# Performance work log

Hardware: AMD Instinct MI355X
Metric: run time of the kernel (lower is better)

## Reference

```python
import jax, jax.numpy as jnp
import numpy as np

L, H = 16384, 1024

def setup_inputs() -> dict:
    key = jax.random.key(0)
    x = jax.random.normal(key, (L, H), dtype=jnp.float32)
    # learned parameter: tau initialized to log(0.8) per channel
    tau = jnp.full((H,), jnp.log(jnp.float32(0.8)), dtype=jnp.float32)
    return {"x": x, "tau": tau}

def _binop(q_i, q_j):
    # diagonal linear recurrence combine: x_j = A_j * x_i + b_j
    A_i, b_i = q_i
    A_j, b_j = q_j
    return (A_j * A_i, A_j * b_i + b_j)

def reference(x, tau):
    # Lambda_bar = exp(tau), B_bar = I  => Bu_elements = x
    Lambda_bar = jnp.exp(tau)                         # (H,)
    B_bar = jnp.eye(x.shape[1], dtype=x.dtype)        # (H, H) identity, as in original
    Bu = jnp.einsum('ph,lh->lp', B_bar, x)            # (L, H) == x
    Lambda_elements = jnp.broadcast_to(Lambda_bar, x.shape)  # (L, H)
    _, xs = jax.lax.associative_scan(_binop, (Lambda_elements, Bu))
    return xs  # (L, H)
```

## Files before the change

kernel.cpp:

```cpp
#include <hip/hip_runtime.h>
#include <cmath>


static constexpr int TC = 16;
static constexpr int P  = 16;

typedef float nt4 __attribute__((ext_vector_type(4)));

__global__ __launch_bounds__(256)
void li_ends(const float4* __restrict__ xv, const float4* __restrict__ tauv,
             float4* __restrict__ ends, int HV) {
    const int t = threadIdx.x;
    const int c = blockIdx.x;
    const float4 tv = tauv[t];
    const float lx = expf(tv.x), ly = expf(tv.y),
                lz = expf(tv.z), lw = expf(tv.w);

    const float4* xp = xv + (size_t)c * TC * HV + t;
    float4 buf[TC];
#pragma unroll
    for (int i = 0; i < TC; ++i)
        buf[i] = xp[(size_t)i * HV];

    float4 s = make_float4(0.f, 0.f, 0.f, 0.f);
#pragma unroll
    for (int i = 0; i < TC; ++i) {
        s.x = fmaf(lx, s.x, buf[i].x);
        s.y = fmaf(ly, s.y, buf[i].y);
        s.z = fmaf(lz, s.z, buf[i].z);
        s.w = fmaf(lw, s.w, buf[i].w);
    }
    ends[(size_t)c * HV + t] = s;
}

__global__ __launch_bounds__(256)
void li_pagg(const float4* __restrict__ ends, const float4* __restrict__ tauv,
             float4* __restrict__ pa, int HV) {
    const int gid = blockIdx.x * 256 + threadIdx.x;
    const int t = gid % HV;
    const int p = gid / HV;
    const float4 tv = tauv[t];
    const float Tx = expf(tv.x * (float)TC), Ty = expf(tv.y * (float)TC),
                Tz = expf(tv.z * (float)TC), Tw = expf(tv.w * (float)TC);

    const float4* ep = ends + (size_t)p * P * HV + t;
    float4 buf[P];
#pragma unroll
    for (int j = 0; j < P; ++j)
        buf[j] = ep[(size_t)j * HV];

    float4 s = make_float4(0.f, 0.f, 0.f, 0.f);
#pragma unroll
    for (int j = 0; j < P; ++j) {
        s.x = fmaf(Tx, s.x, buf[j].x);
        s.y = fmaf(Ty, s.y, buf[j].y);
        s.z = fmaf(Tz, s.z, buf[j].z);
        s.w = fmaf(Tw, s.w, buf[j].w);
    }
    pa[(size_t)p * HV + t] = s;
}

__global__ __launch_bounds__(256)
void li_pscan(float4* __restrict__ pa, const float4* __restrict__ tauv,
              int HV, int NP) {
    const int t = threadIdx.x;
    const float4 tv = tauv[t];
    const float fP = (float)(P * TC);
    const float Px = expf(tv.x * fP), Py = expf(tv.y * fP),
                Pz = expf(tv.z * fP), Pw = expf(tv.w * fP);
    float4 c = make_float4(0.f, 0.f, 0.f, 0.f);
    for (int p0 = 0; p0 < NP; p0 += 16) {
        float4 v[16];
#pragma unroll
        for (int j = 0; j < 16; ++j)
            v[j] = pa[(size_t)(p0 + j) * HV + t];
#pragma unroll
        for (int j = 0; j < 16; ++j) {
            const float4 a = v[j];
            v[j] = c;
            c.x = fmaf(Px, c.x, a.x);
            c.y = fmaf(Py, c.y, a.y);
            c.z = fmaf(Pz, c.z, a.z);
            c.w = fmaf(Pw, c.w, a.w);
        }
#pragma unroll
        for (int j = 0; j < 16; ++j)
            pa[(size_t)(p0 + j) * HV + t] = v[j];
    }
}

__global__ __launch_bounds__(256)
void li_out(const float4* __restrict__ xv, const float4* __restrict__ tauv,
            const float4* __restrict__ ends, const float4* __restrict__ pc,
            float4* __restrict__ yv, int HV) {
    const int t = threadIdx.x;
    const int c = blockIdx.x;
    const int p = c / P;
    const int r = c % P;
    const float4 tv = tauv[t];
    const float lx = expf(tv.x), ly = expf(tv.y),
                lz = expf(tv.z), lw = expf(tv.w);
    const float Tx = expf(tv.x * (float)TC), Ty = expf(tv.y * (float)TC),
                Tz = expf(tv.z * (float)TC), Tw = expf(tv.w * (float)TC);

    float4 carry = pc[(size_t)p * HV + t];
    {
        float4 v[P - 1];
        const float4* ep = ends + (size_t)p * P * HV + t;
#pragma unroll
        for (int j = 0; j < P - 1; ++j)
            if (j < r) v[j] = ep[(size_t)j * HV];
#pragma unroll
        for (int j = 0; j < P - 1; ++j) {
            if (j < r) {
                carry.x = fmaf(Tx, carry.x, v[j].x);
                carry.y = fmaf(Ty, carry.y, v[j].y);
                carry.z = fmaf(Tz, carry.z, v[j].z);
                carry.w = fmaf(Tw, carry.w, v[j].w);
            }
        }
    }

    const size_t base = (size_t)c * TC * HV + t;
    float4 buf[TC];
#pragma unroll
    for (int i = 0; i < TC; ++i)
        buf[i] = xv[base + (size_t)i * HV];

    float4 s = carry;
#pragma unroll
    for (int i = 0; i < TC; ++i) {
        s.x = fmaf(lx, s.x, buf[i].x);
        s.y = fmaf(ly, s.y, buf[i].y);
        s.z = fmaf(lz, s.z, buf[i].z);
        s.w = fmaf(lw, s.w, buf[i].w);
        buf[i] = s;
    }
    nt4* yn = (nt4*)yv;
#pragma unroll
    for (int i = 0; i < TC; ++i) {
        nt4 o = { buf[i].x, buf[i].y, buf[i].z, buf[i].w };
        __builtin_nontemporal_store(o, &yn[base + (size_t)i * HV]);
    }
}

extern "C" void kernel_launch(void* const* d_in, const int* in_sizes, int n_in,
                              void* d_out, int out_size, void* d_ws, size_t ws_size,
                              hipStream_t stream) {
    const float* x   = (const float*)d_in[0];
    const float* tau = (const float*)d_in[1];
    float* y = (float*)d_out;

    const int H  = in_sizes[1];
    const int L  = in_sizes[0] / H;
    const int C  = L / TC;
    const int NP = C / P;
    const int HV = H / 4;

    float4* ends = (float4*)d_ws;
    float4* pa   = ends + (size_t)C * HV;

    const float4* xv   = (const float4*)x;
    const float4* tauv = (const float4*)tau;

    li_ends <<<dim3(C),             dim3(256), 0, stream>>>(xv, tauv, ends, HV);
    li_pagg <<<dim3(NP * HV / 256), dim3(256), 0, stream>>>(ends, tauv, pa, HV);
    li_pscan<<<dim3(1),             dim3(256), 0, stream>>>(pa, tauv, HV, NP);
    li_out  <<<dim3(C),             dim3(256), 0, stream>>>(xv, tauv, ends, pa,
                                                            (float4*)y, HV);
}
```

Before: 132.7 us.

## Fuse scan stages into one cooperative kernel with register-resident chunk data

Replaces the four-kernel pipeline with one cooperative kernel that loads each x chunk once, keeps its local prefix in registers, and uses two grid-wide syncs between the chunk-end, partition-aggregate and output phases. The serial single-block partition scan is replaced by each block summing its preceding partition aggregates directly, and the output is formed as local prefix plus decayed carry, so x is not read a second time. C is 1024 blocks, and the cooperative launch needs all of them resident at once (256 CUs × 4 blocks). If that is not possible it falls back to the old kernels. The costs are grid-sync overhead and redundant carry work that grows with partition index.

```diff
diff --git a/kernel.cpp b/kernel.cpp
--- a/kernel.cpp
+++ b/kernel.cpp
@@ -1,11 +1,131 @@
 #include <hip/hip_runtime.h>
+#include <hip/hip_cooperative_groups.h>
 #include <cmath>
 
+
+namespace cg = cooperative_groups;
 
 static constexpr int TC = 16;
 static constexpr int P  = 16;
 
 typedef float nt4 __attribute__((ext_vector_type(4)));
+
+__device__ inline float4 ntload(const float4* p) {
+    nt4 v = __builtin_nontemporal_load((const nt4*)p);
+    return make_float4(v.x, v.y, v.z, v.w);
+}
+
+__global__ __launch_bounds__(256, 4)
+void li_coop(const float4* __restrict__ xv, const float4* __restrict__ tauv,
+             float4* __restrict__ yv, float4* __restrict__ ends,
+             float4* __restrict__ pa, int HV, int NP)
+{
+    const int t = threadIdx.x;
+    const int c = blockIdx.x;
+
+    const float4 tv = tauv[t];
+    const float lx = expf(tv.x), ly = expf(tv.y),
+                lz = expf(tv.z), lw = expf(tv.w);
+    const float Tx = expf(tv.x * (float)TC), Ty = expf(tv.y * (float)TC),
+                Tz = expf(tv.z * (float)TC), Tw = expf(tv.w * (float)TC);
+    const float fQ = (float)(TC * P);
+    const float Qx = expf(tv.x * fQ), Qy = expf(tv.y * fQ),
+                Qz = expf(tv.z * fQ), Qw = expf(tv.w * fQ);
+
+    const size_t base = (size_t)c * TC * HV + t;
+    float4 buf[TC];
+#pragma unroll
+    for (int i = 0; i < TC; ++i)
+        buf[i] = ntload(&xv[base + (size_t)i * HV]);
+
+    float4 s = make_float4(0.f, 0.f, 0.f, 0.f);
+#pragma unroll
+    for (int i = 0; i < TC; ++i) {
+        s.x = fmaf(lx, s.x, buf[i].x);
+        s.y = fmaf(ly, s.y, buf[i].y);
+        s.z = fmaf(lz, s.z, buf[i].z);
+        s.w = fmaf(lw, s.w, buf[i].w);
+        buf[i] = s;
+    }
+    ends[(size_t)c * HV + t] = s;
+
+    cg::this_grid().sync();
+
+    if (c < NP) {
+        const float4* ep = ends + (size_t)c * P * HV + t;
+        float4 a = make_float4(0.f, 0.f, 0.f, 0.f);
+#pragma unroll
+        for (int j0 = 0; j0 < P; j0 += 8) {
+            float4 v[8];
+#pragma unroll
+            for (int j = 0; j < 8; ++j)
+                v[j] = ep[(size_t)(j0 + j) * HV];
+#pragma unroll
+            for (int j = 0; j < 8; ++j) {
+                a.x = fmaf(Tx, a.x, v[j].x);
+                a.y = fmaf(Ty, a.y, v[j].y);
+                a.z = fmaf(Tz, a.z, v[j].z);
+                a.w = fmaf(Tw, a.w, v[j].w);
+            }
+        }
+        pa[(size_t)c * HV + t] = a;
+    }
+
+    cg::this_grid().sync();
+
+    const int p = c / P;
+    const int r = c % P;
+
+    float4 carry = make_float4(0.f, 0.f, 0.f, 0.f);
+    for (int q0 = 0; q0 < p; q0 += 8) {
+        const int n = p - q0;
+        float4 v[8];
+#pragma unroll
+        for (int j = 0; j < 8; ++j)
+            if (j < n) v[j] = pa[(size_t)(q0 + j) * HV + t];
+#pragma unroll
+        for (int j = 0; j < 8; ++j) {
+            if (j < n) {
+                carry.x = fmaf(Qx, carry.x, v[j].x);
+                carry.y = fmaf(Qy, carry.y, v[j].y);
+                carry.z = fmaf(Qz, carry.z, v[j].z);
+                carry.w = fmaf(Qw, carry.w, v[j].w);
+            }
+        }
+    }
+    {
+        const float4* ep = ends + (size_t)p * P * HV + t;
+        for (int j0 = 0; j0 < r; j0 += 8) {
+            const int n = r - j0;
+            float4 v[8];
+#pragma unroll
+            for (int j = 0; j < 8; ++j)
+                if (j < n) v[j] = ep[(size_t)(j0 + j) * HV];
+#pragma unroll
+            for (int j = 0; j < 8; ++j) {
+                if (j < n) {
+                    carry.x = fmaf(Tx, carry.x, v[j].x);
+                    carry.y = fmaf(Ty, carry.y, v[j].y);
+                    carry.z = fmaf(Tz, carry.z, v[j].z);
+                    carry.w = fmaf(Tw, carry.w, v[j].w);
+                }
+            }
+        }
+    }
+
+    float4 pm = make_float4(lx, ly, lz, lw);
+    nt4* yn = (nt4*)yv;
+#pragma unroll
+    for (int i = 0; i < TC; ++i) {
+        nt4 o = { fmaf(pm.x, carry.x, buf[i].x),
+                  fmaf(pm.y, carry.y, buf[i].y),
+                  fmaf(pm.z, carry.z, buf[i].z),
+                  fmaf(pm.w, carry.w, buf[i].w) };
+        __builtin_nontemporal_store(o, &yn[base + (size_t)i * HV]);
+        pm.x *= lx; pm.y *= ly; pm.z *= lz; pm.w *= lw;
+    }
+}
+
 
 __global__ __launch_bounds__(256)
 void li_ends(const float4* __restrict__ xv, const float4* __restrict__ tauv,
@@ -15,13 +135,11 @@
     const float4 tv = tauv[t];
     const float lx = expf(tv.x), ly = expf(tv.y),
                 lz = expf(tv.z), lw = expf(tv.w);
-
     const float4* xp = xv + (size_t)c * TC * HV + t;
     float4 buf[TC];
 #pragma unroll
     for (int i = 0; i < TC; ++i)
         buf[i] = xp[(size_t)i * HV];
-
     float4 s = make_float4(0.f, 0.f, 0.f, 0.f);
 #pragma unroll
     for (int i = 0; i < TC; ++i) {
@@ -42,13 +160,11 @@
     const float4 tv = tauv[t];
     const float Tx = expf(tv.x * (float)TC), Ty = expf(tv.y * (float)TC),
                 Tz = expf(tv.z * (float)TC), Tw = expf(tv.w * (float)TC);
-
     const float4* ep = ends + (size_t)p * P * HV + t;
     float4 buf[P];
 #pragma unroll
     for (int j = 0; j < P; ++j)
         buf[j] = ep[(size_t)j * HV];
-
     float4 s = make_float4(0.f, 0.f, 0.f, 0.f);
 #pragma unroll
     for (int j = 0; j < P; ++j) {
@@ -102,7 +218,6 @@
                 lz = expf(tv.z), lw = expf(tv.w);
     const float Tx = expf(tv.x * (float)TC), Ty = expf(tv.y * (float)TC),
                 Tz = expf(tv.z * (float)TC), Tw = expf(tv.w * (float)TC);
-
     float4 carry = pc[(size_t)p * HV + t];
     {
         float4 v[P - 1];
@@ -120,13 +235,11 @@
             }
         }
     }
-
     const size_t base = (size_t)c * TC * HV + t;
     float4 buf[TC];
 #pragma unroll
     for (int i = 0; i < TC; ++i)
         buf[i] = xv[base + (size_t)i * HV];
-
     float4 s = carry;
 #pragma unroll
     for (int i = 0; i < TC; ++i) {
@@ -162,10 +275,26 @@
 
     const float4* xv   = (const float4*)x;
     const float4* tauv = (const float4*)tau;
-
-    li_ends <<<dim3(C),             dim3(256), 0, stream>>>(xv, tauv, ends, HV);
-    li_pagg <<<dim3(NP * HV / 256), dim3(256), 0, stream>>>(ends, tauv, pa, HV);
-    li_pscan<<<dim3(1),             dim3(256), 0, stream>>>(pa, tauv, HV, NP);
-    li_out  <<<dim3(C),             dim3(256), 0, stream>>>(xv, tauv, ends, pa,
-                                                            (float4*)y, HV);
-}
+    float4*       yv   = (float4*)y;
+
+    int blocksPerCU = 0;
+    hipError_t qe = hipOccupancyMaxActiveBlocksPerMultiprocessor(
+        &blocksPerCU, li_coop, 256, 0);
+
+    bool coop_ok = false;
+    if (qe == hipSuccess && blocksPerCU >= 4) {
+        void* args[] = { (void*)&xv, (void*)&tauv, (void*)&yv,
+                         (void*)&ends, (void*)&pa, (void*)&HV, (void*)&NP };
+        hipError_t le = hipLaunchCooperativeKernel(
+            li_coop, dim3(C), dim3(256), args, 0u, stream);
+        coop_ok = (le == hipSuccess);
+    }
+
+    if (!coop_ok) {
+        li_ends <<<dim3(C),             dim3(256), 0, stream>>>(xv, tauv, ends, HV);
+        li_pagg <<<dim3(NP * HV / 256), dim3(256), 0, stream>>>(ends, tauv, pa, HV);
+        li_pscan<<<dim3(1),             dim3(256), 0, stream>>>(pa, tauv, HV, NP);
+        li_out  <<<dim3(C),             dim3(256), 0, stream>>>(xv, tauv, ends, pa,
+                                                                yv, HV);
+    }
+}
```

Measured after the change: 131.8 us. Within noise of the previous version (-0.7%).
